# Performance work log

Hardware: AMD Instinct MI355X
Metric: run time of the kernel (lower is better)

Reference implementation:

```python
import jax, jax.numpy as jnp
import numpy as np

N = 100000
IN_DIM = 256
HID = 128
E = 1600000


def _gcn_conv(x, W, b, src, dst, n_nodes):
    """PyG GCNConv: add self-loops, symmetric normalization, linear transform."""
    xw = x @ W  # [N, H]
    loop = jnp.arange(n_nodes, dtype=src.dtype)
    s = jnp.concatenate([src, loop])  # sources (j)
    d = jnp.concatenate([dst, loop])  # targets (i)
    ones = jnp.ones(s.shape[0], dtype=x.dtype)
    deg = jax.ops.segment_sum(ones, d, num_segments=n_nodes)  # in-degree incl. self-loop
    dinv = jnp.where(deg > 0, jax.lax.rsqrt(deg), 0.0)
    norm = dinv[s] * dinv[d]  # [E+N]
    msgs = xw[s] * norm[:, None]  # gather + scale
    out = jax.ops.segment_sum(msgs, d, num_segments=n_nodes)  # scatter-add at targets
    return out + b


def setup_inputs() -> dict:
    key = jax.random.key(0)
    ks = jax.random.split(key, 12)
    x = jax.random.normal(ks[0], (N, IN_DIM), dtype=jnp.float32)
    edge_index = jax.random.randint(ks[1], (2, E), 0, N, dtype=jnp.int64)
    h_node = jax.random.uniform(ks[2], (N,), dtype=jnp.float32)
    # learned params (glorot-ish scale)
    W1 = jax.random.normal(ks[3], (IN_DIM, HID), dtype=jnp.float32) / np.sqrt(IN_DIM)
    b1 = jnp.zeros((HID,), dtype=jnp.float32)
    W2 = jax.random.normal(ks[4], (HID, HID), dtype=jnp.float32) / np.sqrt(HID)
    b2 = jnp.zeros((HID,), dtype=jnp.float32)
    Wc = jax.random.normal(ks[5], (HID, 2), dtype=jnp.float32) / np.sqrt(HID)
    bc = jnp.zeros((2,), dtype=jnp.float32)
    Wf = jax.random.normal(ks[6], (HID, 2), dtype=jnp.float32) / np.sqrt(HID)
    bf = jnp.zeros((2,), dtype=jnp.float32)
    return {"x": x, "edge_index": edge_index, "h_node": h_node,
            "W1": W1, "b1": b1, "W2": W2, "b2": b2,
            "Wc": Wc, "bc": bc, "Wf": Wf, "bf": bf}


def reference(x, edge_index, h_node, W1, b1, W2, b2, Wc, bc, Wf, bf):
    src, dst = edge_index[0], edge_index[1]
    h1 = jax.nn.relu(_gcn_conv(x, W1, b1, src, dst, x.shape[0]))      # [N, HID]
    logits_coarse = h1 @ Wc + bc                                      # [N, 2]
    alpha = h_node[:, None]                                           # [N, 1]
    h2 = jax.nn.relu(_gcn_conv(h1, W2, b2, src, dst, x.shape[0]))     # [N, HID]
    h2_adaptive = alpha * h2 + (1.0 - alpha) * h1
    logits_fine = h2_adaptive @ Wf + bf                               # [N, 2]
    return 0.5 * logits_coarse + 0.5 * logits_fine
```

## Files before the change

kernel.cpp:

```cpp
#include <hip/hip_runtime.h>


#define HID 128
#define SHIFT 9
#define RANGE 512
#define MAXB 256
#define TILE 4096

typedef __bf16 bf16x8 __attribute__((ext_vector_type(8)));
typedef float  f32x4  __attribute__((ext_vector_type(4)));
typedef float  f32x2  __attribute__((ext_vector_type(2)));

__device__ __forceinline__ unsigned short f2bf(float x) {
    unsigned int b = __float_as_uint(x);
    b += 0x7fffu + ((b >> 16) & 1u);
    return (unsigned short)(b >> 16);
}
__device__ __forceinline__ float bflo(unsigned int u) { return __uint_as_float(u << 16); }
__device__ __forceinline__ float bfhi(unsigned int u) { return __uint_as_float(u & 0xffff0000u); }
__device__ __forceinline__ unsigned packbf(float a, float b) {
    return (unsigned)f2bf(a) | ((unsigned)f2bf(b) << 16);
}


__global__ __launch_bounds__(256)
void bincount_kernel(const int* __restrict__ dst, int* __restrict__ bin_counts,
                     int E, int NB) {
    __shared__ int h[MAXB];
    for (int i = threadIdx.x; i < NB; i += 256) h[i] = 0;
    __syncthreads();
    const int base = blockIdx.x * TILE;
#pragma unroll
    for (int j = 0; j < TILE; j += 256) {
        int e = base + j + threadIdx.x;
        if (e < E) atomicAdd(&h[((unsigned)dst[e]) >> SHIFT], 1);
    }
    __syncthreads();
    for (int i = threadIdx.x; i < NB; i += 256) {
        int v = h[i];
        if (v) atomicAdd(&bin_counts[i], v);
    }
}

__global__ void binscan_kernel(const int* __restrict__ bin_counts,
                               int* __restrict__ bin_off, int* __restrict__ bin_cur, int NB) {
    __shared__ int sh[MAXB];
    const int t = threadIdx.x;
    int v = (t < NB) ? bin_counts[t] : 0;
    sh[t] = v;
    __syncthreads();
    for (int s = 1; s < 256; s <<= 1) {
        int x = (t >= s) ? sh[t - s] : 0;
        __syncthreads();
        sh[t] += x;
        __syncthreads();
    }
    if (t < NB) {
        int ex = sh[t] - v;
        bin_off[t] = ex;
        bin_cur[t] = ex;
    }
}

__global__ __launch_bounds__(256)
void stage_kernel(const int* __restrict__ src, const int* __restrict__ dst,
                  int* __restrict__ bin_cur, unsigned* __restrict__ pairs, int E) {
    __shared__ int sh_hist[MAXB];
    __shared__ int sh_off[MAXB];
    __shared__ int sh_ex[MAXB];
    __shared__ int sh_gbase[MAXB];
    __shared__ uint2 stg[TILE];
    const int t = threadIdx.x;
    const int base = blockIdx.x * TILE;
    const int cnt = min(TILE, E - base);

    for (int i = t; i < MAXB; i += 256) sh_hist[i] = 0;
    __syncthreads();

    int s[16], d[16], r[16];
#pragma unroll
    for (int j = 0; j < 16; ++j) {
        const int k = j * 256 + t;
        if (k < cnt) {
            s[j] = src[base + k];
            d[j] = dst[base + k];
            r[j] = atomicAdd(&sh_hist[((unsigned)d[j]) >> SHIFT], 1);
        }
    }
    __syncthreads();

    const int hv = sh_hist[t];
    sh_off[t] = hv;
    __syncthreads();
    for (int st = 1; st < 256; st <<= 1) {
        int x = (t >= st) ? sh_off[t - st] : 0;
        __syncthreads();
        sh_off[t] += x;
        __syncthreads();
    }
    sh_ex[t] = sh_off[t] - hv;
    if (hv > 0) sh_gbase[t] = atomicAdd(&bin_cur[t], hv);
    __syncthreads();

#pragma unroll
    for (int j = 0; j < 16; ++j) {
        const int k = j * 256 + t;
        if (k < cnt) {
            int b = ((unsigned)d[j]) >> SHIFT;
            stg[sh_ex[b] + r[j]] = make_uint2((unsigned)s[j], (unsigned)d[j]);
        }
    }
    __syncthreads();

    for (int i = t; i < cnt; i += 256) {
        uint2 p = stg[i];
        int b = (int)(p.y >> SHIFT);
        unsigned w = ((p.y & (RANGE - 1)) << 23) | p.x;
        pairs[sh_gbase[b] + (i - sh_ex[b])] = w;
    }
}

__global__ __launch_bounds__(256)
void binrowp_kernel(const unsigned* __restrict__ pairs, const int* __restrict__ bin_off,
                    float* __restrict__ dinv, int* __restrict__ rowp,
                    int N, int NB, int E) {
    __shared__ int c[RANGE];
    __shared__ int sh[256];
    const int b = blockIdx.x;
    const int t = threadIdx.x;
    const int nb = b << SHIFT;
    const int nr = min(RANGE, N - nb);
    for (int i = t; i < RANGE; i += 256) c[i] = 0;
    __syncthreads();
    const int lo = bin_off[b];
    const int hi = (b + 1 < NB) ? bin_off[b + 1] : E;
    for (int i = lo + t; i < hi; i += 256)
        atomicAdd(&c[pairs[i] >> 23], 1);
    __syncthreads();
    const int v0 = c[2 * t], v1 = c[2 * t + 1];
    const int pr = v0 + v1;
    sh[t] = pr;
    __syncthreads();
    for (int s = 1; s < 256; s <<= 1) {
        int x = (t >= s) ? sh[t - s] : 0;
        __syncthreads();
        sh[t] += x;
        __syncthreads();
    }
    const int ex = sh[t] - pr + lo;
    if (2 * t < nr) {
        rowp[nb + 2 * t] = ex;
        dinv[nb + 2 * t] = rsqrtf((float)(v0 + 1));
    }
    if (2 * t + 1 < nr) {
        rowp[nb + 2 * t + 1] = ex + v0;
        dinv[nb + 2 * t + 1] = rsqrtf((float)(v1 + 1));
    }
    if (b == 0 && t == 0) rowp[N] = E;
}

__global__ __launch_bounds__(256)
void fine_kernel(const unsigned* __restrict__ pairs, const int* __restrict__ bin_off,
                 const int* __restrict__ rowp, const float* __restrict__ dinv,
                 unsigned* __restrict__ colv1, int N, int NB, int E) {
    __shared__ int cur[RANGE];
    const int b = blockIdx.x;
    const int nb = b << SHIFT;
    const int nr = min(RANGE, N - nb);
    for (int i = threadIdx.x; i < nr; i += 256) cur[i] = rowp[nb + i];
    __syncthreads();
    const int lo = bin_off[b];
    const int hi = (b + 1 < NB) ? bin_off[b + 1] : E;
    for (int i = lo + threadIdx.x; i < hi; i += 256) {
        unsigned w = pairs[i];
        unsigned s = w & 0x7fffffu;
        int pos = atomicAdd(&cur[w >> 23], 1);
        unsigned w15 = __float2uint_rn(dinv[s] * 32767.0f);
        colv1[pos] = (s << 15) | w15;
    }
}

__global__ void prep_kernel(const float* __restrict__ W1, const float* __restrict__ W2,
                            unsigned short* __restrict__ wt1, unsigned short* __restrict__ wt2,
                            int K1, int* __restrict__ bin_counts) {
    int idx = blockIdx.x * 256 + threadIdx.x;
    if (idx < MAXB) bin_counts[idx] = 0;
    if (idx < 128 * K1) {
        int nn = idx / K1, k = idx - nn * K1;
        wt1[(size_t)nn * K1 + k] = f2bf(W1[(size_t)k * 128 + nn]);
    }
    if (idx < 128 * 128) {
        int nn = idx >> 7, k = idx & 127;
        wt2[(size_t)nn * 128 + k] = f2bf(W2[(size_t)k * 128 + nn]);
    }
}

template <bool A_BF16, int K>
__global__ __launch_bounds__(256)
void gemm_kernel(const void* __restrict__ Aptr, const unsigned short* __restrict__ Wt,
                 unsigned short* __restrict__ Out, int nrows) {
    constexpr int NIT = K / 32;
    constexpr int DEPTH = (NIT < 4) ? NIT : 4;
    const int tid  = threadIdx.x;
    const int wave = tid >> 6;
    const int lane = tid & 63;
    const int q = lane >> 4;
    const int r = lane & 15;
    const int wrow = blockIdx.x * 128 + wave * 32;
    const size_t row0 = (size_t)min(wrow + r,      nrows - 1);
    const size_t row1 = (size_t)min(wrow + 16 + r, nrows - 1);

    const unsigned short* A16 = (const unsigned short*)Aptr;
    const float*          A32 = (const float*)Aptr;

    f32x4 acc[2][8];
#pragma unroll
    for (int s = 0; s < 2; ++s)
#pragma unroll
        for (int c = 0; c < 8; ++c) acc[s][c] = (f32x4){0.f, 0.f, 0.f, 0.f};

    bf16x8 preb[DEPTH][2];
    float4 pref[DEPTH][2][2];

#pragma unroll
    for (int i = 0; i < DEPTH; ++i) {
        const int kk = i * 32 + q * 8;
        if (A_BF16) {
            preb[i][0] = *reinterpret_cast<const bf16x8*>(A16 + row0 * K + kk);
            preb[i][1] = *reinterpret_cast<const bf16x8*>(A16 + row1 * K + kk);
        } else {
            pref[i][0][0] = *reinterpret_cast<const float4*>(A32 + row0 * K + kk);
            pref[i][0][1] = *reinterpret_cast<const float4*>(A32 + row0 * K + kk + 4);
            pref[i][1][0] = *reinterpret_cast<const float4*>(A32 + row1 * K + kk);
            pref[i][1][1] = *reinterpret_cast<const float4*>(A32 + row1 * K + kk + 4);
        }
    }

#pragma unroll
    for (int it = 0; it < NIT; ++it) {
        const int slot = it % DEPTH;
        const int kk = it * 32 + q * 8;

        bf16x8 bfr[8];
#pragma unroll
        for (int c = 0; c < 8; ++c)
            bfr[c] = *reinterpret_cast<const bf16x8*>(Wt + (size_t)(c * 16 + r) * K + kk);

        bf16x8 afrag[2];
#pragma unroll
        for (int s = 0; s < 2; ++s) {
            if (A_BF16) {
                afrag[s] = preb[slot][s];
            } else {
                const float4 x0 = pref[slot][s][0];
                const float4 x1 = pref[slot][s][1];
                bf16x8 a;
                a[0] = (__bf16)x0.x; a[1] = (__bf16)x0.y; a[2] = (__bf16)x0.z; a[3] = (__bf16)x0.w;
                a[4] = (__bf16)x1.x; a[5] = (__bf16)x1.y; a[6] = (__bf16)x1.z; a[7] = (__bf16)x1.w;
                afrag[s] = a;
            }
        }

        if (it + DEPTH < NIT) {
            const int kk2 = (it + DEPTH) * 32 + q * 8;
            if (A_BF16) {
                preb[slot][0] = *reinterpret_cast<const bf16x8*>(A16 + row0 * K + kk2);
                preb[slot][1] = *reinterpret_cast<const bf16x8*>(A16 + row1 * K + kk2);
            } else {
                pref[slot][0][0] = *reinterpret_cast<const float4*>(A32 + row0 * K + kk2);
                pref[slot][0][1] = *reinterpret_cast<const float4*>(A32 + row0 * K + kk2 + 4);
                pref[slot][1][0] = *reinterpret_cast<const float4*>(A32 + row1 * K + kk2);
                pref[slot][1][1] = *reinterpret_cast<const float4*>(A32 + row1 * K + kk2 + 4);
            }
        }

#pragma unroll
        for (int c = 0; c < 8; ++c) {
            acc[0][c] = __builtin_amdgcn_mfma_f32_16x16x32_bf16(afrag[0], bfr[c], acc[0][c], 0, 0, 0);
            acc[1][c] = __builtin_amdgcn_mfma_f32_16x16x32_bf16(afrag[1], bfr[c], acc[1][c], 0, 0, 0);
        }
    }

#pragma unroll
    for (int s = 0; s < 2; ++s)
#pragma unroll
        for (int v = 0; v < 4; ++v) {
            const int row = wrow + s * 16 + q * 4 + v;
            if (row < nrows) {
#pragma unroll
                for (int c = 0; c < 8; ++c)
                    Out[(size_t)row * 128 + c * 16 + r] = f2bf(acc[s][c][v]);
            }
        }
}


#define AGG_EDGE_LOOP(XW)                                                      \
    for (int base = beg; base < end; base += 64) {                             \
        const int e = base + lane;                                             \
        const unsigned cw = (e < end) ? colv1[e] : 0u;                         \
        const int cnt = min(64, end - base);                                   \
        _Pragma("unroll 4")                                                    \
        for (int t = 0; t < cnt; t += 4) {                                     \
            const unsigned cg = (unsigned)__shfl((int)cw, t + q4);             \
            const unsigned st = cg >> 15;                                      \
            const float    wt = (float)(cg & 0x7fffu) * (1.0f / 32767.0f);     \
            const uint4 uu = *reinterpret_cast<const uint4*>(                  \
                (const char*)(XW) + ((st << 8) + coff));                       \
            A0 += (f32x2){bflo(uu.x), bfhi(uu.x)} * wt;                        \
            A1 += (f32x2){bflo(uu.y), bfhi(uu.y)} * wt;                        \
            A2 += (f32x2){bflo(uu.z), bfhi(uu.z)} * wt;                        \
            A3 += (f32x2){bflo(uu.w), bfhi(uu.w)} * wt;                        \
        }                                                                      \
    }                                                                          \
    A0 += __shfl_xor(A0, 16); A1 += __shfl_xor(A1, 16);                        \
    A2 += __shfl_xor(A2, 16); A3 += __shfl_xor(A3, 16);                        \
    A0 += __shfl_xor(A0, 32); A1 += __shfl_xor(A1, 32);                        \
    A2 += __shfl_xor(A2, 32); A3 += __shfl_xor(A3, 32);

__device__ __forceinline__ f32x2 __shfl_xor(f32x2 v, int m) {
    return (f32x2){__shfl_xor(v[0], m), __shfl_xor(v[1], m)};
}

__global__ __launch_bounds__(256)
void agg1_kernel(const unsigned short* __restrict__ xw, const unsigned* __restrict__ colv1,
                 const int* __restrict__ rowp, const float* __restrict__ dinv,
                 const float* __restrict__ b1, const float* __restrict__ Wc,
                 const float* __restrict__ bc, uint4* __restrict__ h1,
                 float* __restrict__ outp, int n) {
    const int node = blockIdx.x * 4 + (threadIdx.x >> 6);
    if (node >= n) return;
    const int lane = threadIdx.x & 63;
    const int c    = lane & 15;
    const int q4   = lane >> 4;
    const unsigned coff = (unsigned)c << 4;
    const float di = dinv[node];

    f32x2 A0 = {0.f,0.f}, A1 = {0.f,0.f}, A2 = {0.f,0.f}, A3 = {0.f,0.f};
    {
        const float ws = (q4 == 0) ? di : 0.f;
        const uint4 uu = *reinterpret_cast<const uint4*>(
            (const char*)xw + (((unsigned)node << 8) + coff));
        A0 += (f32x2){bflo(uu.x), bfhi(uu.x)} * ws;
        A1 += (f32x2){bflo(uu.y), bfhi(uu.y)} * ws;
        A2 += (f32x2){bflo(uu.z), bfhi(uu.z)} * ws;
        A3 += (f32x2){bflo(uu.w), bfhi(uu.w)} * ws;
    }

    const int beg = rowp[node], end = rowp[node + 1];
    AGG_EDGE_LOOP(xw)

    const float4 bb0 = reinterpret_cast<const float4*>(b1)[2*c];
    const float4 bb1 = reinterpret_cast<const float4*>(b1)[2*c + 1];
    float a0 = fmaxf(A0[0]*di + bb0.x, 0.f), a1 = fmaxf(A0[1]*di + bb0.y, 0.f);
    float a2 = fmaxf(A1[0]*di + bb0.z, 0.f), a3 = fmaxf(A1[1]*di + bb0.w, 0.f);
    float a4 = fmaxf(A2[0]*di + bb1.x, 0.f), a5 = fmaxf(A2[1]*di + bb1.y, 0.f);
    float a6 = fmaxf(A3[0]*di + bb1.z, 0.f), a7 = fmaxf(A3[1]*di + bb1.w, 0.f);

    if (q4 == 0)
        h1[((unsigned)node << 4) + c] =
            make_uint4(packbf(a0,a1), packbf(a2,a3), packbf(a4,a5), packbf(a6,a7));

    const float4 w0 = reinterpret_cast<const float4*>(Wc)[4*c];
    const float4 w1 = reinterpret_cast<const float4*>(Wc)[4*c + 1];
    const float4 w2 = reinterpret_cast<const float4*>(Wc)[4*c + 2];
    const float4 w3 = reinterpret_cast<const float4*>(Wc)[4*c + 3];
    float c0 = a0*w0.x + a1*w0.z + a2*w1.x + a3*w1.z
             + a4*w2.x + a5*w2.z + a6*w3.x + a7*w3.z;
    float c1 = a0*w0.y + a1*w0.w + a2*w1.y + a3*w1.w
             + a4*w2.y + a5*w2.w + a6*w3.y + a7*w3.w;
    if (q4) { c0 = 0.f; c1 = 0.f; }
#pragma unroll
    for (int off = 32; off; off >>= 1) {
        c0 += __shfl_down(c0, off);
        c1 += __shfl_down(c1, off);
    }
    if (lane == 0) {
        outp[2 * (size_t)node]     = 0.5f * (c0 + bc[0]);
        outp[2 * (size_t)node + 1] = 0.5f * (c1 + bc[1]);
    }
}

__global__ __launch_bounds__(256)
void agg2_kernel(const unsigned short* __restrict__ xw2, const uint4* __restrict__ h1,
                 const unsigned* __restrict__ colv1, const int* __restrict__ rowp,
                 const float* __restrict__ dinv, const float* __restrict__ b2,
                 const float* __restrict__ Wf, const float* __restrict__ bfv,
                 const float* __restrict__ hnode, float* __restrict__ outp, int n) {
    const int node = blockIdx.x * 4 + (threadIdx.x >> 6);
    if (node >= n) return;
    const int lane = threadIdx.x & 63;
    const int c    = lane & 15;
    const int q4   = lane >> 4;
    const unsigned coff = (unsigned)c << 4;
    const float di = dinv[node];

    f32x2 A0 = {0.f,0.f}, A1 = {0.f,0.f}, A2 = {0.f,0.f}, A3 = {0.f,0.f};
    {
        const float ws = (q4 == 0) ? di : 0.f;
        const uint4 uu = *reinterpret_cast<const uint4*>(
            (const char*)xw2 + (((unsigned)node << 8) + coff));
        A0 += (f32x2){bflo(uu.x), bfhi(uu.x)} * ws;
        A1 += (f32x2){bflo(uu.y), bfhi(uu.y)} * ws;
        A2 += (f32x2){bflo(uu.z), bfhi(uu.z)} * ws;
        A3 += (f32x2){bflo(uu.w), bfhi(uu.w)} * ws;
    }

    const int beg = rowp[node], end = rowp[node + 1];
    AGG_EDGE_LOOP(xw2)

    const float4 bb0 = reinterpret_cast<const float4*>(b2)[2*c];
    const float4 bb1 = reinterpret_cast<const float4*>(b2)[2*c + 1];
    float h20 = fmaxf(A0[0]*di + bb0.x, 0.f), h21 = fmaxf(A0[1]*di + bb0.y, 0.f);
    float h22 = fmaxf(A1[0]*di + bb0.z, 0.f), h23 = fmaxf(A1[1]*di + bb0.w, 0.f);
    float h24 = fmaxf(A2[0]*di + bb1.x, 0.f), h25 = fmaxf(A2[1]*di + bb1.y, 0.f);
    float h26 = fmaxf(A3[0]*di + bb1.z, 0.f), h27 = fmaxf(A3[1]*di + bb1.w, 0.f);

    const float alpha = hnode[node];
    const float beta  = 1.f - alpha;
    const uint4 hh = h1[((unsigned)node << 4) + c];
    const float ha0 = alpha*h20 + beta*bflo(hh.x);
    const float ha1 = alpha*h21 + beta*bfhi(hh.x);
    const float ha2 = alpha*h22 + beta*bflo(hh.y);
    const float ha3 = alpha*h23 + beta*bfhi(hh.y);
    const float ha4 = alpha*h24 + beta*bflo(hh.z);
    const float ha5 = alpha*h25 + beta*bfhi(hh.z);
    const float ha6 = alpha*h26 + beta*bflo(hh.w);
    const float ha7 = alpha*h27 + beta*bfhi(hh.w);

    const float4 w0 = reinterpret_cast<const float4*>(Wf)[4*c];
    const float4 w1 = reinterpret_cast<const float4*>(Wf)[4*c + 1];
    const float4 w2 = reinterpret_cast<const float4*>(Wf)[4*c + 2];
    const float4 w3 = reinterpret_cast<const float4*>(Wf)[4*c + 3];
    float f0 = ha0*w0.x + ha1*w0.z + ha2*w1.x + ha3*w1.z
             + ha4*w2.x + ha5*w2.z + ha6*w3.x + ha7*w3.z;
    float f1 = ha0*w0.y + ha1*w0.w + ha2*w1.y + ha3*w1.w
             + ha4*w2.y + ha5*w2.w + ha6*w3.y + ha7*w3.w;
    if (q4) { f0 = 0.f; f1 = 0.f; }
#pragma unroll
    for (int off = 32; off; off >>= 1) {
        f0 += __shfl_down(f0, off);
        f1 += __shfl_down(f1, off);
    }
    if (lane == 0) {
        outp[2 * (size_t)node]     += 0.5f * (f0 + bfv[0]);
        outp[2 * (size_t)node + 1] += 0.5f * (f1 + bfv[1]);
    }
}


extern "C" void kernel_launch(void* const* d_in, const int* in_sizes, int n_in,
                              void* d_out, int out_size, void* d_ws, size_t ws_size,
                              hipStream_t stream) {
    const float* x     = (const float*)d_in[0];
    const int*   ei    = (const int*)d_in[1];
    const float* hnode = (const float*)d_in[2];
    const float* W1    = (const float*)d_in[3];
    const float* b1    = (const float*)d_in[4];
    const float* W2    = (const float*)d_in[5];
    const float* b2    = (const float*)d_in[6];
    const float* Wc    = (const float*)d_in[7];
    const float* bc    = (const float*)d_in[8];
    const float* Wf    = (const float*)d_in[9];
    const float* bfv   = (const float*)d_in[10];

    const int N  = in_sizes[2];
    const int E  = in_sizes[1] / 2;
    const int K1 = in_sizes[3] / HID;
    const int NB = (N + RANGE - 1) >> SHIFT;
    const int* srcv = ei;
    const int* dstv = ei + E;
    float* outp = (float*)d_out;

    char* ws = (char*)d_ws;
    size_t off = 0;
    auto alloc = [&](size_t bytes) -> char* {
        char* p = ws + off;
        off += (bytes + 255) & ~(size_t)255;
        return p;
    };
    unsigned short* xw       = (unsigned short*)alloc((size_t)N * HID * 2);
    unsigned short* h1       = (unsigned short*)alloc((size_t)N * HID * 2);
    float*          dinv     = (float*)alloc((size_t)N * 4);
    int*            rowp     = (int*)alloc((size_t)(N + 1) * 4);
    unsigned*       colv1    = (unsigned*)alloc((size_t)E * 4);
    unsigned*       pairs    = (unsigned*)alloc((size_t)E * 4);
    int*            bin_counts = (int*)alloc(MAXB * 4);
    int*            bin_off    = (int*)alloc(MAXB * 4);
    int*            bin_cur    = (int*)alloc(MAXB * 4);
    unsigned short* wt1      = (unsigned short*)alloc((size_t)HID * K1 * 2);
    unsigned short* wt2      = (unsigned short*)alloc((size_t)HID * HID * 2);

    prep_kernel<<<(HID * K1 + 255) / 256, 256, 0, stream>>>(W1, W2, wt1, wt2, K1, bin_counts);

    const int ntiles = (E + TILE - 1) / TILE;
    bincount_kernel<<<ntiles, 256, 0, stream>>>(dstv, bin_counts, E, NB);
    binscan_kernel<<<1, 256, 0, stream>>>(bin_counts, bin_off, bin_cur, NB);
    stage_kernel<<<ntiles, 256, 0, stream>>>(srcv, dstv, bin_cur, pairs, E);
    binrowp_kernel<<<NB, 256, 0, stream>>>(pairs, bin_off, dinv, rowp, N, NB, E);
    fine_kernel<<<NB, 256, 0, stream>>>(pairs, bin_off, rowp, dinv, colv1, N, NB, E);

    gemm_kernel<false, 256><<<(N + 127) / 128, 256, 0, stream>>>((const void*)x, wt1, xw, N);
    agg1_kernel<<<(N + 3) / 4, 256, 0, stream>>>(xw, colv1, rowp, dinv,
                                                 b1, Wc, bc, (uint4*)h1, outp, N);
    gemm_kernel<true, 128><<<(N + 127) / 128, 256, 0, stream>>>((const void*)h1, wt2, xw, N);
    agg2_kernel<<<(N + 3) / 4, 256, 0, stream>>>(xw, (const uint4*)h1, colv1,
                                                 rowp, dinv, b2, Wf, bfv, hnode, outp, N);
}
```

Measured before the change: 432.8 us.

## Fuse independent preprocessing stages into combined kernels with block-range dispatch

Merges the x-to-bf16 conversion, weight transposes and the edge bincount into one launch, and runs the edge staging pass alongside the first GEMM in a second launch, with each block choosing its role from its block index. The first GEMM now reads a pre-converted bf16 copy of x instead of converting fp32 inline. The aim is fewer launches and overlap of the memory-bound edge sort with the compute-heavy GEMM. The cost is an extra bf16 copy of x that is written and then read back, plus shared-memory and register demand set by the larger role in each fused kernel, which may reduce occupancy.

Result: no change. 435.7 us (+0.7%).

```diff
diff --git a/kernel.cpp b/kernel.cpp
--- a/kernel.cpp
+++ b/kernel.cpp
@@ -23,13 +23,12 @@
 }
 
 
-__global__ __launch_bounds__(256)
-void bincount_kernel(const int* __restrict__ dst, int* __restrict__ bin_counts,
-                     int E, int NB) {
+__device__ void bincount_body(int blk, const int* __restrict__ dst,
+                              int* __restrict__ bin_counts, int E, int NB) {
     __shared__ int h[MAXB];
     for (int i = threadIdx.x; i < NB; i += 256) h[i] = 0;
     __syncthreads();
-    const int base = blockIdx.x * TILE;
+    const int base = blk * TILE;
 #pragma unroll
     for (int j = 0; j < TILE; j += 256) {
         int e = base + j + threadIdx.x;
@@ -62,16 +61,15 @@
     }
 }
 
-__global__ __launch_bounds__(256)
-void stage_kernel(const int* __restrict__ src, const int* __restrict__ dst,
-                  int* __restrict__ bin_cur, unsigned* __restrict__ pairs, int E) {
+__device__ void stage_body(int blk, const int* __restrict__ src, const int* __restrict__ dst,
+                           int* __restrict__ bin_cur, unsigned* __restrict__ pairs, int E) {
     __shared__ int sh_hist[MAXB];
     __shared__ int sh_off[MAXB];
     __shared__ int sh_ex[MAXB];
     __shared__ int sh_gbase[MAXB];
     __shared__ uint2 stg[TILE];
     const int t = threadIdx.x;
-    const int base = blockIdx.x * TILE;
+    const int base = blk * TILE;
     const int cnt = min(TILE, E - base);
 
     for (int i = t; i < MAXB; i += 256) sh_hist[i] = 0;
@@ -180,25 +178,10 @@
     }
 }
 
-__global__ void prep_kernel(const float* __restrict__ W1, const float* __restrict__ W2,
-                            unsigned short* __restrict__ wt1, unsigned short* __restrict__ wt2,
-                            int K1, int* __restrict__ bin_counts) {
-    int idx = blockIdx.x * 256 + threadIdx.x;
-    if (idx < MAXB) bin_counts[idx] = 0;
-    if (idx < 128 * K1) {
-        int nn = idx / K1, k = idx - nn * K1;
-        wt1[(size_t)nn * K1 + k] = f2bf(W1[(size_t)k * 128 + nn]);
-    }
-    if (idx < 128 * 128) {
-        int nn = idx >> 7, k = idx & 127;
-        wt2[(size_t)nn * 128 + k] = f2bf(W2[(size_t)k * 128 + nn]);
-    }
-}
-
-template <bool A_BF16, int K>
-__global__ __launch_bounds__(256)
-void gemm_kernel(const void* __restrict__ Aptr, const unsigned short* __restrict__ Wt,
-                 unsigned short* __restrict__ Out, int nrows) {
+template <int K>
+__device__ void gemm_body(int blk, const unsigned short* __restrict__ A16,
+                          const unsigned short* __restrict__ Wt,
+                          unsigned short* __restrict__ Out, int nrows) {
     constexpr int NIT = K / 32;
     constexpr int DEPTH = (NIT < 4) ? NIT : 4;
     const int tid  = threadIdx.x;
@@ -206,13 +189,10 @@
     const int lane = tid & 63;
     const int q = lane >> 4;
     const int r = lane & 15;
-    const int wrow = blockIdx.x * 128 + wave * 32;
+    const int wrow = blk * 128 + wave * 32;
     const size_t row0 = (size_t)min(wrow + r,      nrows - 1);
     const size_t row1 = (size_t)min(wrow + 16 + r, nrows - 1);
 
-    const unsigned short* A16 = (const unsigned short*)Aptr;
-    const float*          A32 = (const float*)Aptr;
-
     f32x4 acc[2][8];
 #pragma unroll
     for (int s = 0; s < 2; ++s)
@@ -220,20 +200,11 @@
         for (int c = 0; c < 8; ++c) acc[s][c] = (f32x4){0.f, 0.f, 0.f, 0.f};
 
     bf16x8 preb[DEPTH][2];
-    float4 pref[DEPTH][2][2];
-
 #pragma unroll
     for (int i = 0; i < DEPTH; ++i) {
         const int kk = i * 32 + q * 8;
-        if (A_BF16) {
-            preb[i][0] = *reinterpret_cast<const bf16x8*>(A16 + row0 * K + kk);
-            preb[i][1] = *reinterpret_cast<const bf16x8*>(A16 + row1 * K + kk);
-        } else {
-            pref[i][0][0] = *reinterpret_cast<const float4*>(A32 + row0 * K + kk);
-            pref[i][0][1] = *reinterpret_cast<const float4*>(A32 + row0 * K + kk + 4);
-            pref[i][1][0] = *reinterpret_cast<const float4*>(A32 + row1 * K + kk);
-            pref[i][1][1] = *reinterpret_cast<const float4*>(A32 + row1 * K + kk + 4);
-        }
+        preb[i][0] = *reinterpret_cast<const bf16x8*>(A16 + row0 * K + kk);
+        preb[i][1] = *reinterpret_cast<const bf16x8*>(A16 + row1 * K + kk);
     }
 
 #pragma unroll
@@ -246,38 +217,19 @@
         for (int c = 0; c < 8; ++c)
             bfr[c] = *reinterpret_cast<const bf16x8*>(Wt + (size_t)(c * 16 + r) * K + kk);
 
-        bf16x8 afrag[2];
-#pragma unroll
-        for (int s = 0; s < 2; ++s) {
-            if (A_BF16) {
-                afrag[s] = preb[slot][s];
-            } else {
-                const float4 x0 = pref[slot][s][0];
-                const float4 x1 = pref[slot][s][1];
-                bf16x8 a;
-                a[0] = (__bf16)x0.x; a[1] = (__bf16)x0.y; a[2] = (__bf16)x0.z; a[3] = (__bf16)x0.w;
-                a[4] = (__bf16)x1.x; a[5] = (__bf16)x1.y; a[6] = (__bf16)x1.z; a[7] = (__bf16)x1.w;
-                afrag[s] = a;
-            }
-        }
+        const bf16x8 a0 = preb[slot][0];
+        const bf16x8 a1 = preb[slot][1];
 
         if (it + DEPTH < NIT) {
             const int kk2 = (it + DEPTH) * 32 + q * 8;
-            if (A_BF16) {
-                preb[slot][0] = *reinterpret_cast<const bf16x8*>(A16 + row0 * K + kk2);
-                preb[slot][1] = *reinterpret_cast<const bf16x8*>(A16 + row1 * K + kk2);
-            } else {
-                pref[slot][0][0] = *reinterpret_cast<const float4*>(A32 + row0 * K + kk2);
-                pref[slot][0][1] = *reinterpret_cast<const float4*>(A32 + row0 * K + kk2 + 4);
-                pref[slot][1][0] = *reinterpret_cast<const float4*>(A32 + row1 * K + kk2);
-                pref[slot][1][1] = *reinterpret_cast<const float4*>(A32 + row1 * K + kk2 + 4);
-            }
+            preb[slot][0] = *reinterpret_cast<const bf16x8*>(A16 + row0 * K + kk2);
+            preb[slot][1] = *reinterpret_cast<const bf16x8*>(A16 + row1 * K + kk2);
         }
 
 #pragma unroll
         for (int c = 0; c < 8; ++c) {
-            acc[0][c] = __builtin_amdgcn_mfma_f32_16x16x32_bf16(afrag[0], bfr[c], acc[0][c], 0, 0, 0);
-            acc[1][c] = __builtin_amdgcn_mfma_f32_16x16x32_bf16(afrag[1], bfr[c], acc[1][c], 0, 0, 0);
+            acc[0][c] = __builtin_amdgcn_mfma_f32_16x16x32_bf16(a0, bfr[c], acc[0][c], 0, 0, 0);
+            acc[1][c] = __builtin_amdgcn_mfma_f32_16x16x32_bf16(a1, bfr[c], acc[1][c], 0, 0, 0);
         }
     }
 
@@ -292,6 +244,65 @@
                     Out[(size_t)row * 128 + c * 16 + r] = f2bf(acc[s][c][v]);
             }
         }
+}
+
+
+__global__ __launch_bounds__(256)
+void d1_kernel(const float* __restrict__ x, unsigned short* __restrict__ xbf,
+               long long NK,
+               const float* __restrict__ W1, const float* __restrict__ W2,
+               unsigned short* __restrict__ wt1, unsigned short* __restrict__ wt2,
+               int K1, const int* __restrict__ dst, int* __restrict__ bin_counts,
+               int E, int NB, int ncb, int nb1, int nb2) {
+    const int b = blockIdx.x;
+    const int tid = threadIdx.x;
+    if (b < ncb) {
+        const long long base = ((long long)b * 256 + tid) * 8;
+        if (base + 8 <= NK) {
+            const float4 x0 = *reinterpret_cast<const float4*>(x + base);
+            const float4 x1 = *reinterpret_cast<const float4*>(x + base + 4);
+            uint4 o;
+            o.x = packbf(x0.x, x0.y); o.y = packbf(x0.z, x0.w);
+            o.z = packbf(x1.x, x1.y); o.w = packbf(x1.z, x1.w);
+            *reinterpret_cast<uint4*>(xbf + base) = o;
+        } else {
+            for (long long i = base; i < NK; ++i) xbf[i] = f2bf(x[i]);
+        }
+    } else if (b < ncb + nb1) {
+        int idx = (b - ncb) * 256 + tid;
+        if (idx < 128 * K1) {
+            int nn = idx / K1, k = idx - nn * K1;
+            wt1[(size_t)nn * K1 + k] = f2bf(W1[(size_t)k * 128 + nn]);
+        }
+    } else if (b < ncb + nb1 + nb2) {
+        int idx = (b - ncb - nb1) * 256 + tid;
+        if (idx < 128 * 128) {
+            int nn = idx >> 7, k = idx & 127;
+            wt2[(size_t)nn * 128 + k] = f2bf(W2[(size_t)k * 128 + nn]);
+        }
+    } else {
+        bincount_body(b - ncb - nb1 - nb2, dst, bin_counts, E, NB);
+    }
+}
+
+
+__global__ __launch_bounds__(256)
+void d3_kernel(const int* __restrict__ src, const int* __restrict__ dst,
+               int* __restrict__ bin_cur, unsigned* __restrict__ pairs, int E,
+               int ntiles, const unsigned short* __restrict__ xbf,
+               const unsigned short* __restrict__ wt1,
+               unsigned short* __restrict__ xw, int nrows) {
+    if ((int)blockIdx.x < ntiles)
+        stage_body(blockIdx.x, src, dst, bin_cur, pairs, E);
+    else
+        gemm_body<256>(blockIdx.x - ntiles, xbf, wt1, xw, nrows);
+}
+
+__global__ __launch_bounds__(256)
+void gemm2_kernel(const unsigned short* __restrict__ A,
+                  const unsigned short* __restrict__ Wt,
+                  unsigned short* __restrict__ Out, int nrows) {
+    gemm_body<128>(blockIdx.x, A, Wt, Out, nrows);
 }
 
 
@@ -479,6 +490,7 @@
         off += (bytes + 255) & ~(size_t)255;
         return p;
     };
+    unsigned short* xbf      = (unsigned short*)alloc((size_t)N * K1 * 2);
     unsigned short* xw       = (unsigned short*)alloc((size_t)N * HID * 2);
     unsigned short* h1       = (unsigned short*)alloc((size_t)N * HID * 2);
     float*          dinv     = (float*)alloc((size_t)N * 4);
@@ -491,19 +503,29 @@
     unsigned short* wt1      = (unsigned short*)alloc((size_t)HID * K1 * 2);
     unsigned short* wt2      = (unsigned short*)alloc((size_t)HID * HID * 2);
 
-    prep_kernel<<<(HID * K1 + 255) / 256, 256, 0, stream>>>(W1, W2, wt1, wt2, K1, bin_counts);
-
+    const long long NK = (long long)N * K1;
+    const int ncb = (int)((NK + 2047) / 2048);
+    const int nb1 = (128 * K1 + 255) / 256;
+    const int nb2 = (128 * 128 + 255) / 256;
     const int ntiles = (E + TILE - 1) / TILE;
-    bincount_kernel<<<ntiles, 256, 0, stream>>>(dstv, bin_counts, E, NB);
+    const int ngemm  = (N + 127) / 128;
+
+    hipMemsetAsync(bin_counts, 0, MAXB * 4, stream);
+
+    d1_kernel<<<ncb + nb1 + nb2 + ntiles, 256, 0, stream>>>(
+        x, xbf, NK, W1, W2, wt1, wt2, K1, dstv, bin_counts, E, NB, ncb, nb1, nb2);
+
     binscan_kernel<<<1, 256, 0, stream>>>(bin_counts, bin_off, bin_cur, NB);
-    stage_kernel<<<ntiles, 256, 0, stream>>>(srcv, dstv, bin_cur, pairs, E);
+
+    d3_kernel<<<ntiles + ngemm, 256, 0, stream>>>(
+        srcv, dstv, bin_cur, pairs, E, ntiles, xbf, wt1, xw, N);
+
     binrowp_kernel<<<NB, 256, 0, stream>>>(pairs, bin_off, dinv, rowp, N, NB, E);
     fine_kernel<<<NB, 256, 0, stream>>>(pairs, bin_off, rowp, dinv, colv1, N, NB, E);
 
-    gemm_kernel<false, 256><<<(N + 127) / 128, 256, 0, stream>>>((const void*)x, wt1, xw, N);
     agg1_kernel<<<(N + 3) / 4, 256, 0, stream>>>(xw, colv1, rowp, dinv,
                                                  b1, Wc, bc, (uint4*)h1, outp, N);
-    gemm_kernel<true, 128><<<(N + 127) / 128, 256, 0, stream>>>((const void*)h1, wt2, xw, N);
+    gemm2_kernel<<<ngemm, 256, 0, stream>>>(h1, wt2, xw, N);
     agg2_kernel<<<(N + 3) / 4, 256, 0, stream>>>(xw, (const uint4*)h1, colv1,
                                                  rowp, dinv, b2, Wf, bfv, hnode, outp, N);
 }
```
